# Performance work log

Measured on AMD Instinct MI355X. Metric: run time of the kernel, lower is better.

Reference implementation:

```python
import jax, jax.numpy as jnp
import numpy as np

B, M, N = 1, 8192, 131072      # batch, bones, window points
C_BOT, C = 16, 128             # bottleneck_channel, channel
K_MAX, FOLD, R_UP = 8, 8, 4    # max neighbors, fold_channel, upsample rate r
EPS = 1e-8


def _lin_init(key, fan_in, fan_out):
    return jax.random.normal(key, (fan_in, fan_out), jnp.float32) / np.sqrt(fan_in)


def setup_inputs() -> dict:
    key = jax.random.key(0)
    ks = jax.random.split(key, 10)
    return {
        "quantized_cf": jax.random.normal(ks[0], (B, M, C_BOT), jnp.float32),
        "d_idx": jax.random.randint(ks[1], (B, N, K_MAX), 0, M),
        "d_windows": jax.random.normal(ks[2], (B, N, 3), jnp.float32),
        "bones": jax.random.normal(ks[3], (B, M, 3), jnp.float32),
        "K": 8,
        # fea_stretch Linear(bottleneck -> channel)
        "W_stretch": _lin_init(ks[4], C_BOT, C),
        "b_stretch": jnp.zeros((C,), jnp.float32),
        # DWUS folding MLP: (C+3) -> C -> FOLD*R_UP -> 3 (per fold point)
        "W1": _lin_init(ks[5], C + 3, C),
        "b1": jnp.zeros((C,), jnp.float32),
        "W2": _lin_init(ks[6], C, FOLD * R_UP),
        "b2": jnp.zeros((FOLD * R_UP,), jnp.float32),
        "W3": _lin_init(ks[7], FOLD, 3),
        "b3": jnp.zeros((3,), jnp.float32),
    }


def reference(quantized_cf, d_idx, d_windows, bones, K,
              W_stretch, b_stretch, W1, b1, W2, b2, W3, b3):
    # fea_stretch: per-bone feature expansion  [B, M, C]
    skin_fea = jnp.einsum("bmc,cd->bmd", quantized_cf, W_stretch) + b_stretch

    idx = d_idx[..., :K]                                   # [B, N, K]
    batch = jnp.arange(B)[:, None, None]
    g_fea = skin_fea[batch, idx]                           # [B, N, K, C] gather
    g_bones = bones[batch, idx]                            # [B, N, K, 3]

    # inverse-distance interpolation of bone features onto window points
    rel = d_windows[:, :, None, :] - g_bones               # [B, N, K, 3]
    dist = jnp.sqrt(jnp.sum(rel * rel, axis=-1) + EPS)     # [B, N, K]
    w = 1.0 / (dist + EPS)
    w = w / jnp.sum(w, axis=-1, keepdims=True)
    interp = jnp.einsum("bnk,bnkc->bnc", w, g_fea)         # [B, N, C]

    # folding-based upsampling: each window point emits R_UP refined points
    x = jnp.concatenate([interp, d_windows], axis=-1)      # [B, N, C+3]
    h = jax.nn.relu(jnp.einsum("bnc,cd->bnd", x, W1) + b1)
    h = jax.nn.relu(jnp.einsum("bnc,cd->bnd", h, W2) + b2)
    h = h.reshape(B, N, R_UP, FOLD)
    off = jnp.einsum("bnrf,fo->bnro", h, W3) + b3          # [B, N, R_UP, 3]
    rec = d_windows[:, :, None, :] + off                   # [B, N, R_UP, 3]
    return rec.reshape(B, N * R_UP, 3)
```

## Files before the change

kernel.cpp:

```cpp
#include <hip/hip_runtime.h>
#include <hip/hip_bf16.h>

typedef __attribute__((ext_vector_type(8))) short short8;
typedef __attribute__((ext_vector_type(4))) float f32x4;

#define NPTS 131072

__device__ inline unsigned short f2bf(float f) {
    unsigned u = __float_as_uint(f);
    u = (u + 0x7FFFu + ((u >> 16) & 1u)) >> 16;
    return (unsigned short)u;
}

__device__ inline unsigned pack2(float a, float b) {
    union { __hip_bfloat162 h; unsigned u; } v;
    v.h = __float22bfloat162_rn(float2{a, b});
    return v.u;
}

__global__ __launch_bounds__(256) void prep_kernel(
    const float* __restrict__ Ws, const float* __restrict__ bs,
    const float* __restrict__ W1, const float* __restrict__ b1,
    const float* __restrict__ W2, const float* __restrict__ W3,
    const float* __restrict__ bones,
    unsigned short* __restrict__ w1t, unsigned short* __restrict__ w2t,
    float* __restrict__ beff, unsigned short* __restrict__ w3t,
    float* __restrict__ bones4)
{
    int t = blockIdx.x * 256 + threadIdx.x;
    if (t < 4096) {
        int e = t >> 5, k = t & 31;
        float v = 0.f;
        if (k < 16) {
            for (int d = 0; d < 128; ++d) v = fmaf(Ws[k*128 + d], W1[d*128 + e], v);
        } else if (k < 19) {
            v = W1[(128 + (k - 16))*128 + e];
        }
        w1t[e*32 + k] = f2bf(v);
    } else if (t < 8192) {
        int t2 = t - 4096;
        int e = t2 >> 7, d = t2 & 127;
        w2t[e*128 + ((d & 15)*8 + (d >> 4))] = f2bf(W2[d*32 + e]);
    } else if (t < 8320) {
        int e = t - 8192;
        float v = b1[e];
        for (int d = 0; d < 128; ++d) v = fmaf(bs[d], W1[d*128 + e], v);
        beff[e] = v;
    } else if (t < 8832) {
        int i = t - 8320;
        int q = i >> 5, k = i & 31;
        int e = (k & 1)*16 + (k >> 1);
        int r = e >> 3, f = e & 7;
        float v = 0.f;
        if (q < 12) {
            int r2 = q / 3, o = q - r2*3;
            if (r == r2) v = W3[f*3 + o];
        }
        w3t[q*32 + k] = f2bf(v);
    } else if (t < 8832 + 4*8192) {
        int i = t - 8832;
        int id = i >> 2, c = i & 3;
        bones4[i] = (c < 3) ? bones[id*3 + c] : 0.f;
    }
}

#define WREG 5632

__global__ __launch_bounds__(256, 3) void decoder_kernel(
    const float* __restrict__ qcf, const int* __restrict__ didx,
    const float* __restrict__ dwin, const float* __restrict__ bones4,
    const unsigned short* __restrict__ w1t, const unsigned short* __restrict__ w2t,
    const float* __restrict__ beff, const float* __restrict__ b2,
    const unsigned short* __restrict__ w3t, const float* __restrict__ b3,
    float* __restrict__ out)
{
    __shared__ unsigned char lds[4 * WREG];

    const int tid  = threadIdx.x;
    const int wave = tid >> 6;
    const int lane = tid & 63;
    unsigned char* wbase = lds + wave * WREG;
    unsigned short* H1b = (unsigned short*)(wbase);
    unsigned short* H2p = (unsigned short*)(wbase + 4352);

    const int q4  = lane >> 4;
    const int l16 = lane & 15;

    const int gw   = blockIdx.x * 4 + wave;
    const int base = gw * 16;
    const int p    = base + l16;

    const int4 ia = *(const int4*)(didx + p*8);
    const int4 ib = *(const int4*)(didx + p*8 + 4);
    const int id[8] = { ia.x, ia.y, ia.z, ia.w, ib.x, ib.y, ib.z, ib.w };
    const float wx = dwin[p*3+0], wy = dwin[p*3+1], wz = dwin[p*3+2];

    const int o3c = l16 - (l16/3)*3;
    float rw0 = 0.f, rw1 = 0.f, rw2 = 0.f, rw3 = 0.f;
    if (l16 < 12) {
        rw0 = dwin[(size_t)(base + q4*4 + 0)*3 + o3c];
        rw1 = dwin[(size_t)(base + q4*4 + 1)*3 + o3c];
        rw2 = dwin[(size_t)(base + q4*4 + 2)*3 + o3c];
        rw3 = dwin[(size_t)(base + q4*4 + 3)*3 + o3c];
    }

    const float4* __restrict__ bn4 = (const float4*)bones4;
    float w[8]; float s = 0.f;
#pragma unroll
    for (int k = 0; k < 8; ++k) {
        const float4 b = bn4[id[k]];
        const float rx = wx - b.x, ry = wy - b.y, rz = wz - b.z;
        const float dist = sqrtf(fmaf(rx,rx, fmaf(ry,ry, fmaf(rz,rz, 1e-8f))));
        w[k] = 1.0f / (dist + 1e-8f);
        s += w[k];
    }
    const float inv = 1.0f / s;

    union { unsigned u[4]; short8 s8; } a1u;
    a1u.u[0] = a1u.u[1] = a1u.u[2] = a1u.u[3] = 0u;
    if (q4 < 2) {
        float acc[8] = {0.f,0.f,0.f,0.f,0.f,0.f,0.f,0.f};
        const float4* __restrict__ q4p = (const float4*)qcf;
#pragma unroll
        for (int k = 0; k < 8; ++k) {
            const float4 lo = q4p[id[k]*4 + q4*2 + 0];
            const float4 hi = q4p[id[k]*4 + q4*2 + 1];
            acc[0] = fmaf(w[k], lo.x, acc[0]);
            acc[1] = fmaf(w[k], lo.y, acc[1]);
            acc[2] = fmaf(w[k], lo.z, acc[2]);
            acc[3] = fmaf(w[k], lo.w, acc[3]);
            acc[4] = fmaf(w[k], hi.x, acc[4]);
            acc[5] = fmaf(w[k], hi.y, acc[5]);
            acc[6] = fmaf(w[k], hi.z, acc[6]);
            acc[7] = fmaf(w[k], hi.w, acc[7]);
        }
        a1u.u[0] = pack2(acc[0]*inv, acc[1]*inv);
        a1u.u[1] = pack2(acc[2]*inv, acc[3]*inv);
        a1u.u[2] = pack2(acc[4]*inv, acc[5]*inv);
        a1u.u[3] = pack2(acc[6]*inv, acc[7]*inv);
    } else if (q4 == 2) {
        a1u.u[0] = pack2(wx, wy);
        a1u.u[1] = pack2(wz, 0.f);
    }

    short8 W1f[8]; float beffv[8];
#pragma unroll
    for (int dt = 0; dt < 8; ++dt) {
        W1f[dt]   = *(const short8*)(w1t + (dt*16 + l16)*32 + q4*8);
        beffv[dt] = beff[dt*16 + l16];
    }
    short8 W2f[2][4]; float b2v[2];
#pragma unroll
    for (int et = 0; et < 2; ++et) {
        b2v[et] = b2[et*16 + l16];
#pragma unroll
        for (int kt = 0; kt < 4; ++kt)
            W2f[et][kt] = *(const short8*)(w2t + (et*16 + l16)*128 + kt*32 + q4*8);
    }
    const short8 w3f = *(const short8*)(w3t + l16*32 + q4*8);
    const float  b3o = (l16 < 12) ? b3[o3c] : 0.f;

    f32x4 acc1[8];
#pragma unroll
    for (int dt = 0; dt < 8; ++dt) {
        f32x4 c = { beffv[dt], beffv[dt], beffv[dt], beffv[dt] };
        acc1[dt] = __builtin_amdgcn_mfma_f32_16x16x32_bf16(a1u.s8, W1f[dt], c, 0, 0, 0);
    }
#pragma unroll
    for (int r = 0; r < 4; ++r) {
        union { unsigned u[4]; short8 s8; } pk;
        pk.u[0] = pack2(fmaxf(acc1[0][r],0.f), fmaxf(acc1[1][r],0.f));
        pk.u[1] = pack2(fmaxf(acc1[2][r],0.f), fmaxf(acc1[3][r],0.f));
        pk.u[2] = pack2(fmaxf(acc1[4][r],0.f), fmaxf(acc1[5][r],0.f));
        pk.u[3] = pack2(fmaxf(acc1[6][r],0.f), fmaxf(acc1[7][r],0.f));
        *(short8*)(H1b + (q4*4 + r)*136 + l16*8) = pk.s8;
    }
    __syncthreads();

    f32x4 acc2[2] = { { b2v[0], b2v[0], b2v[0], b2v[0] },
                      { b2v[1], b2v[1], b2v[1], b2v[1] } };
#pragma unroll
    for (int kt = 0; kt < 4; ++kt) {
        const short8 a2 = *(const short8*)(H1b + l16*136 + kt*32 + q4*8);
        acc2[0] = __builtin_amdgcn_mfma_f32_16x16x32_bf16(a2, W2f[0][kt], acc2[0], 0, 0, 0);
        acc2[1] = __builtin_amdgcn_mfma_f32_16x16x32_bf16(a2, W2f[1][kt], acc2[1], 0, 0, 0);
    }
#pragma unroll
    for (int r = 0; r < 4; ++r) {
        unsigned p01 = pack2(fmaxf(acc2[0][r],0.f), fmaxf(acc2[1][r],0.f));
        *(unsigned*)(H2p + (q4*4 + r)*40 + l16*2) = p01;
    }
    __syncthreads();

    const short8 a3 = *(const short8*)(H2p + l16*40 + q4*8);
    f32x4 c3 = { b3o, b3o, b3o, b3o };
    f32x4 o3 = __builtin_amdgcn_mfma_f32_16x16x32_bf16(a3, w3f, c3, 0, 0, 0);
    if (l16 < 12) {
        out[(size_t)(base + q4*4 + 0)*12 + l16] = rw0 + o3[0];
        out[(size_t)(base + q4*4 + 1)*12 + l16] = rw1 + o3[1];
        out[(size_t)(base + q4*4 + 2)*12 + l16] = rw2 + o3[2];
        out[(size_t)(base + q4*4 + 3)*12 + l16] = rw3 + o3[3];
    }
}

extern "C" void kernel_launch(void* const* d_in, const int* in_sizes, int n_in,
                              void* d_out, int out_size, void* d_ws, size_t ws_size,
                              hipStream_t stream) {
    const float* qcf   = (const float*)d_in[0];
    const int*   didx  = (const int*)  d_in[1];
    const float* dwin  = (const float*)d_in[2];
    const float* bones = (const float*)d_in[3];
    const float* Ws = (const float*)d_in[5];
    const float* bs = (const float*)d_in[6];
    const float* W1 = (const float*)d_in[7];
    const float* b1 = (const float*)d_in[8];
    const float* W2 = (const float*)d_in[9];
    const float* b2 = (const float*)d_in[10];
    const float* W3 = (const float*)d_in[11];
    const float* b3 = (const float*)d_in[12];
    float* out = (float*)d_out;

    unsigned short* w1t    = (unsigned short*)d_ws;
    unsigned short* w2t    = (unsigned short*)((char*)d_ws + 8192);
    float*          beff   = (float*)((char*)d_ws + 16384);
    unsigned short* w3t    = (unsigned short*)((char*)d_ws + 16896);
    float*          bones4 = (float*)((char*)d_ws + 17920);

    hipLaunchKernelGGL(prep_kernel, dim3(163), dim3(256), 0, stream,
                       Ws, bs, W1, b1, W2, W3, bones, w1t, w2t, beff, w3t, bones4);
    hipLaunchKernelGGL(decoder_kernel, dim3(2048), dim3(256), 0, stream,
                       qcf, didx, dwin, bones4, w1t, w2t, beff, b2, w3t, b3, out);
}
```

Before: 35.19 us.

## Process two point tiles per wave to amortize weight fragment loads

Each wave now handles two 16-point tiles, loading the W1/W2/W3 bf16 fragments and biases once and reusing them for both, with the decoder grid halved. The bones padding in the prep kernel writes one float4 per thread instead of one scalar, so the prep grid shrinks. This cuts redundant weight-fragment loads and launch/block overhead, but gives fewer blocks and less parallelism. The two tiles are processed one after the other, so latency hiding may drop.

```diff
diff --git a/kernel.cpp b/kernel.cpp
--- a/kernel.cpp
+++ b/kernel.cpp
@@ -57,54 +57,35 @@
             if (r == r2) v = W3[f*3 + o];
         }
         w3t[q*32 + k] = f2bf(v);
-    } else if (t < 8832 + 4*8192) {
+    } else if (t < 8832 + 8192) {
         int i = t - 8832;
-        int id = i >> 2, c = i & 3;
-        bones4[i] = (c < 3) ? bones[id*3 + c] : 0.f;
+        float4 v;
+        v.x = bones[i*3 + 0];
+        v.y = bones[i*3 + 1];
+        v.z = bones[i*3 + 2];
+        v.w = 0.f;
+        ((float4*)bones4)[i] = v;
     }
 }
 
 #define WREG 5632
 
-__global__ __launch_bounds__(256, 3) void decoder_kernel(
-    const float* __restrict__ qcf, const int* __restrict__ didx,
-    const float* __restrict__ dwin, const float* __restrict__ bones4,
-    const unsigned short* __restrict__ w1t, const unsigned short* __restrict__ w2t,
-    const float* __restrict__ beff, const float* __restrict__ b2,
-    const unsigned short* __restrict__ w3t, const float* __restrict__ b3,
-    float* __restrict__ out)
+struct Frags {
+    short8 W1f[8]; float beffv[8];
+    short8 W2f[2][4]; float b2v[2];
+    short8 w3f; float b3o;
+};
+
+__device__ __forceinline__ void do_tile(
+    int base, const int4 ia, const int4 ib,
+    float wx, float wy, float wz,
+    float rw0, float rw1, float rw2, float rw3,
+    const Frags& F, int q4, int l16,
+    const float4* __restrict__ bn4, const float4* __restrict__ q4p,
+    unsigned short* H1b, unsigned short* H2p, float* __restrict__ out)
 {
-    __shared__ unsigned char lds[4 * WREG];
-
-    const int tid  = threadIdx.x;
-    const int wave = tid >> 6;
-    const int lane = tid & 63;
-    unsigned char* wbase = lds + wave * WREG;
-    unsigned short* H1b = (unsigned short*)(wbase);
-    unsigned short* H2p = (unsigned short*)(wbase + 4352);
-
-    const int q4  = lane >> 4;
-    const int l16 = lane & 15;
-
-    const int gw   = blockIdx.x * 4 + wave;
-    const int base = gw * 16;
-    const int p    = base + l16;
-
-    const int4 ia = *(const int4*)(didx + p*8);
-    const int4 ib = *(const int4*)(didx + p*8 + 4);
     const int id[8] = { ia.x, ia.y, ia.z, ia.w, ib.x, ib.y, ib.z, ib.w };
-    const float wx = dwin[p*3+0], wy = dwin[p*3+1], wz = dwin[p*3+2];
-
-    const int o3c = l16 - (l16/3)*3;
-    float rw0 = 0.f, rw1 = 0.f, rw2 = 0.f, rw3 = 0.f;
-    if (l16 < 12) {
-        rw0 = dwin[(size_t)(base + q4*4 + 0)*3 + o3c];
-        rw1 = dwin[(size_t)(base + q4*4 + 1)*3 + o3c];
-        rw2 = dwin[(size_t)(base + q4*4 + 2)*3 + o3c];
-        rw3 = dwin[(size_t)(base + q4*4 + 3)*3 + o3c];
-    }
-
-    const float4* __restrict__ bn4 = (const float4*)bones4;
+
     float w[8]; float s = 0.f;
 #pragma unroll
     for (int k = 0; k < 8; ++k) {
@@ -120,7 +101,6 @@
     a1u.u[0] = a1u.u[1] = a1u.u[2] = a1u.u[3] = 0u;
     if (q4 < 2) {
         float acc[8] = {0.f,0.f,0.f,0.f,0.f,0.f,0.f,0.f};
-        const float4* __restrict__ q4p = (const float4*)qcf;
 #pragma unroll
         for (int k = 0; k < 8; ++k) {
             const float4 lo = q4p[id[k]*4 + q4*2 + 0];
@@ -143,28 +123,11 @@
         a1u.u[1] = pack2(wz, 0.f);
     }
 
-    short8 W1f[8]; float beffv[8];
+    f32x4 acc1[8];
 #pragma unroll
     for (int dt = 0; dt < 8; ++dt) {
-        W1f[dt]   = *(const short8*)(w1t + (dt*16 + l16)*32 + q4*8);
-        beffv[dt] = beff[dt*16 + l16];
-    }
-    short8 W2f[2][4]; float b2v[2];
-#pragma unroll
-    for (int et = 0; et < 2; ++et) {
-        b2v[et] = b2[et*16 + l16];
-#pragma unroll
-        for (int kt = 0; kt < 4; ++kt)
-            W2f[et][kt] = *(const short8*)(w2t + (et*16 + l16)*128 + kt*32 + q4*8);
-    }
-    const short8 w3f = *(const short8*)(w3t + l16*32 + q4*8);
-    const float  b3o = (l16 < 12) ? b3[o3c] : 0.f;
-
-    f32x4 acc1[8];
-#pragma unroll
-    for (int dt = 0; dt < 8; ++dt) {
-        f32x4 c = { beffv[dt], beffv[dt], beffv[dt], beffv[dt] };
-        acc1[dt] = __builtin_amdgcn_mfma_f32_16x16x32_bf16(a1u.s8, W1f[dt], c, 0, 0, 0);
+        f32x4 c = { F.beffv[dt], F.beffv[dt], F.beffv[dt], F.beffv[dt] };
+        acc1[dt] = __builtin_amdgcn_mfma_f32_16x16x32_bf16(a1u.s8, F.W1f[dt], c, 0, 0, 0);
     }
 #pragma unroll
     for (int r = 0; r < 4; ++r) {
@@ -177,13 +140,13 @@
     }
     __syncthreads();
 
-    f32x4 acc2[2] = { { b2v[0], b2v[0], b2v[0], b2v[0] },
-                      { b2v[1], b2v[1], b2v[1], b2v[1] } };
+    f32x4 acc2[2] = { { F.b2v[0], F.b2v[0], F.b2v[0], F.b2v[0] },
+                      { F.b2v[1], F.b2v[1], F.b2v[1], F.b2v[1] } };
 #pragma unroll
     for (int kt = 0; kt < 4; ++kt) {
         const short8 a2 = *(const short8*)(H1b + l16*136 + kt*32 + q4*8);
-        acc2[0] = __builtin_amdgcn_mfma_f32_16x16x32_bf16(a2, W2f[0][kt], acc2[0], 0, 0, 0);
-        acc2[1] = __builtin_amdgcn_mfma_f32_16x16x32_bf16(a2, W2f[1][kt], acc2[1], 0, 0, 0);
+        acc2[0] = __builtin_amdgcn_mfma_f32_16x16x32_bf16(a2, F.W2f[0][kt], acc2[0], 0, 0, 0);
+        acc2[1] = __builtin_amdgcn_mfma_f32_16x16x32_bf16(a2, F.W2f[1][kt], acc2[1], 0, 0, 0);
     }
 #pragma unroll
     for (int r = 0; r < 4; ++r) {
@@ -193,14 +156,86 @@
     __syncthreads();
 
     const short8 a3 = *(const short8*)(H2p + l16*40 + q4*8);
-    f32x4 c3 = { b3o, b3o, b3o, b3o };
-    f32x4 o3 = __builtin_amdgcn_mfma_f32_16x16x32_bf16(a3, w3f, c3, 0, 0, 0);
+    f32x4 c3 = { F.b3o, F.b3o, F.b3o, F.b3o };
+    f32x4 o3 = __builtin_amdgcn_mfma_f32_16x16x32_bf16(a3, F.w3f, c3, 0, 0, 0);
     if (l16 < 12) {
         out[(size_t)(base + q4*4 + 0)*12 + l16] = rw0 + o3[0];
         out[(size_t)(base + q4*4 + 1)*12 + l16] = rw1 + o3[1];
         out[(size_t)(base + q4*4 + 2)*12 + l16] = rw2 + o3[2];
         out[(size_t)(base + q4*4 + 3)*12 + l16] = rw3 + o3[3];
     }
+}
+
+__global__ __launch_bounds__(256, 3) void decoder_kernel(
+    const float* __restrict__ qcf, const int* __restrict__ didx,
+    const float* __restrict__ dwin, const float* __restrict__ bones4,
+    const unsigned short* __restrict__ w1t, const unsigned short* __restrict__ w2t,
+    const float* __restrict__ beff, const float* __restrict__ b2,
+    const unsigned short* __restrict__ w3t, const float* __restrict__ b3,
+    float* __restrict__ out)
+{
+    __shared__ unsigned char lds[4 * WREG];
+
+    const int tid  = threadIdx.x;
+    const int wave = tid >> 6;
+    const int lane = tid & 63;
+    unsigned char* wbase = lds + wave * WREG;
+    unsigned short* H1b = (unsigned short*)(wbase);
+    unsigned short* H2p = (unsigned short*)(wbase + 4352);
+
+    const int q4  = lane >> 4;
+    const int l16 = lane & 15;
+
+    const int g0    = (blockIdx.x * 4 + wave) * 2;
+    const int base0 = g0 * 16;
+    const int base1 = base0 + 16;
+    const int p0    = base0 + l16;
+    const int p1    = base1 + l16;
+
+    const int4 ia0 = *(const int4*)(didx + p0*8);
+    const int4 ib0 = *(const int4*)(didx + p0*8 + 4);
+    const int4 ia1 = *(const int4*)(didx + p1*8);
+    const int4 ib1 = *(const int4*)(didx + p1*8 + 4);
+    const float wx0 = dwin[p0*3+0], wy0 = dwin[p0*3+1], wz0 = dwin[p0*3+2];
+    const float wx1 = dwin[p1*3+0], wy1 = dwin[p1*3+1], wz1 = dwin[p1*3+2];
+
+    const int o3c = l16 - (l16/3)*3;
+    float rwA0=0.f, rwA1=0.f, rwA2=0.f, rwA3=0.f;
+    float rwB0=0.f, rwB1=0.f, rwB2=0.f, rwB3=0.f;
+    if (l16 < 12) {
+        rwA0 = dwin[(size_t)(base0 + q4*4 + 0)*3 + o3c];
+        rwA1 = dwin[(size_t)(base0 + q4*4 + 1)*3 + o3c];
+        rwA2 = dwin[(size_t)(base0 + q4*4 + 2)*3 + o3c];
+        rwA3 = dwin[(size_t)(base0 + q4*4 + 3)*3 + o3c];
+        rwB0 = dwin[(size_t)(base1 + q4*4 + 0)*3 + o3c];
+        rwB1 = dwin[(size_t)(base1 + q4*4 + 1)*3 + o3c];
+        rwB2 = dwin[(size_t)(base1 + q4*4 + 2)*3 + o3c];
+        rwB3 = dwin[(size_t)(base1 + q4*4 + 3)*3 + o3c];
+    }
+
+    Frags F;
+#pragma unroll
+    for (int dt = 0; dt < 8; ++dt) {
+        F.W1f[dt]   = *(const short8*)(w1t + (dt*16 + l16)*32 + q4*8);
+        F.beffv[dt] = beff[dt*16 + l16];
+    }
+#pragma unroll
+    for (int et = 0; et < 2; ++et) {
+        F.b2v[et] = b2[et*16 + l16];
+#pragma unroll
+        for (int kt = 0; kt < 4; ++kt)
+            F.W2f[et][kt] = *(const short8*)(w2t + (et*16 + l16)*128 + kt*32 + q4*8);
+    }
+    F.w3f = *(const short8*)(w3t + l16*32 + q4*8);
+    F.b3o = (l16 < 12) ? b3[o3c] : 0.f;
+
+    const float4* __restrict__ bn4 = (const float4*)bones4;
+    const float4* __restrict__ q4p = (const float4*)qcf;
+
+    do_tile(base0, ia0, ib0, wx0, wy0, wz0, rwA0, rwA1, rwA2, rwA3,
+            F, q4, l16, bn4, q4p, H1b, H2p, out);
+    do_tile(base1, ia1, ib1, wx1, wy1, wz1, rwB0, rwB1, rwB2, rwB3,
+            F, q4, l16, bn4, q4p, H1b, H2p, out);
 }
 
 extern "C" void kernel_launch(void* const* d_in, const int* in_sizes, int n_in,
@@ -226,8 +261,8 @@
     unsigned short* w3t    = (unsigned short*)((char*)d_ws + 16896);
     float*          bones4 = (float*)((char*)d_ws + 17920);
 
-    hipLaunchKernelGGL(prep_kernel, dim3(163), dim3(256), 0, stream,
+    hipLaunchKernelGGL(prep_kernel, dim3(67), dim3(256), 0, stream,
                        Ws, bs, W1, b1, W2, W3, bones, w1t, w2t, beff, w3t, bones4);
-    hipLaunchKernelGGL(decoder_kernel, dim3(2048), dim3(256), 0, stream,
+    hipLaunchKernelGGL(decoder_kernel, dim3(1024), dim3(256), 0, stream,
                        qcf, didx, dwin, bones4, w1t, w2t, beff, b2, w3t, b3, out);
 }
```

New measurement: 41.07 us. 16.7% more time.

## Spread neighbor gathers across lanes and pre-convert features to bf16

Applied to the files above, without the earlier changes.

The interpolation is restructured so each lane handles one (point, neighbor) pair. Weights are normalized and the feature reduction is done with xor-shuffle butterflies, and the interpolated rows are staged in LDS before the first MFMA. The prep kernel now also converts quantized features to packed bf16, which halves gather bytes, and writes bones4 with float4 stores. The goal is better lane utilization and memory-level parallelism in the gather phase, which previously had only two quarter-waves doing the feature loads. The cost is an extra LDS round-trip and barrier, more shuffles, and an occupancy hint lowered from 3 to 2.

```diff
diff --git a/kernel.cpp b/kernel.cpp
--- a/kernel.cpp
+++ b/kernel.cpp
@@ -18,20 +18,24 @@
     return v.u;
 }
 
+__device__ inline float bflo(unsigned u) { return __uint_as_float(u << 16); }
+__device__ inline float bfhi(unsigned u) { return __uint_as_float(u & 0xffff0000u); }
+
 __global__ __launch_bounds__(256) void prep_kernel(
     const float* __restrict__ Ws, const float* __restrict__ bs,
     const float* __restrict__ W1, const float* __restrict__ b1,
     const float* __restrict__ W2, const float* __restrict__ W3,
-    const float* __restrict__ bones,
+    const float* __restrict__ bones, const float* __restrict__ qcf,
     unsigned short* __restrict__ w1t, unsigned short* __restrict__ w2t,
     float* __restrict__ beff, unsigned short* __restrict__ w3t,
-    float* __restrict__ bones4)
+    float* __restrict__ bones4, unsigned* __restrict__ qbf)
 {
     int t = blockIdx.x * 256 + threadIdx.x;
     if (t < 4096) {
         int e = t >> 5, k = t & 31;
         float v = 0.f;
         if (k < 16) {
+#pragma unroll 16
             for (int d = 0; d < 128; ++d) v = fmaf(Ws[k*128 + d], W1[d*128 + e], v);
         } else if (k < 19) {
             v = W1[(128 + (k - 16))*128 + e];
@@ -44,6 +48,7 @@
     } else if (t < 8320) {
         int e = t - 8192;
         float v = b1[e];
+#pragma unroll 16
         for (int d = 0; d < 128; ++d) v = fmaf(bs[d], W1[d*128 + e], v);
         beff[e] = v;
     } else if (t < 8832) {
@@ -57,17 +62,79 @@
             if (r == r2) v = W3[f*3 + o];
         }
         w3t[q*32 + k] = f2bf(v);
-    } else if (t < 8832 + 4*8192) {
+    } else if (t < 17024) {
         int i = t - 8832;
-        int id = i >> 2, c = i & 3;
-        bones4[i] = (c < 3) ? bones[id*3 + c] : 0.f;
-    }
-}
-
-#define WREG 5632
-
-__global__ __launch_bounds__(256, 3) void decoder_kernel(
-    const float* __restrict__ qcf, const int* __restrict__ didx,
+        float4 v;
+        v.x = bones[i*3 + 0];
+        v.y = bones[i*3 + 1];
+        v.z = bones[i*3 + 2];
+        v.w = 0.f;
+        ((float4*)bones4)[i] = v;
+    } else if (t < 25216) {
+        int row = t - 17024;
+        const float4* q = (const float4*)(qcf + row*16);
+        const float4 q0 = q[0], q1 = q[1], q2 = q[2], q3 = q[3];
+        uint4 o0, o1;
+        o0.x = pack2(q0.x, q0.y); o0.y = pack2(q0.z, q0.w);
+        o0.z = pack2(q1.x, q1.y); o0.w = pack2(q1.z, q1.w);
+        o1.x = pack2(q2.x, q2.y); o1.y = pack2(q2.z, q2.w);
+        o1.z = pack2(q3.x, q3.y); o1.w = pack2(q3.z, q3.w);
+        ((uint4*)qbf)[row*2 + 0] = o0;
+        ((uint4*)qbf)[row*2 + 1] = o1;
+    }
+}
+
+#define WREG 6144
+
+__device__ __forceinline__ float2 interp_pass(
+    int idxv, float4 bb, float wxx, float wyy, float wzz, int k,
+    const unsigned* __restrict__ qbf)
+{
+    const uint4 ra = *(const uint4*)(qbf + idxv*8);
+    const uint4 rb = *(const uint4*)(qbf + idxv*8 + 4);
+
+    const float rx = wxx - bb.x, ry = wyy - bb.y, rz = wzz - bb.z;
+    const float dist = sqrtf(fmaf(rx,rx, fmaf(ry,ry, fmaf(rz,rz, 1e-8f))));
+    const float w = 1.0f / (dist + 1e-8f);
+    float s = w;
+    s += __shfl_xor(s, 1);
+    s += __shfl_xor(s, 2);
+    s += __shfl_xor(s, 4);
+    const float wn = w / s;
+
+    float v[16];
+    v[ 0] = wn*bflo(ra.x); v[ 1] = wn*bfhi(ra.x);
+    v[ 2] = wn*bflo(ra.y); v[ 3] = wn*bfhi(ra.y);
+    v[ 4] = wn*bflo(ra.z); v[ 5] = wn*bfhi(ra.z);
+    v[ 6] = wn*bflo(ra.w); v[ 7] = wn*bfhi(ra.w);
+    v[ 8] = wn*bflo(rb.x); v[ 9] = wn*bfhi(rb.x);
+    v[10] = wn*bflo(rb.y); v[11] = wn*bfhi(rb.y);
+    v[12] = wn*bflo(rb.z); v[13] = wn*bfhi(rb.z);
+    v[14] = wn*bflo(rb.w); v[15] = wn*bfhi(rb.w);
+
+#pragma unroll
+    for (int j = 0; j < 8; ++j) {
+        const float sv = (k & 4) ? v[j] : v[j + 8];
+        const float t  = __shfl_xor(sv, 4);
+        v[j] = ((k & 4) ? v[j + 8] : v[j]) + t;
+    }
+#pragma unroll
+    for (int j = 0; j < 4; ++j) {
+        const float sv = (k & 2) ? v[j] : v[j + 4];
+        const float t  = __shfl_xor(sv, 2);
+        v[j] = ((k & 2) ? v[j + 4] : v[j]) + t;
+    }
+#pragma unroll
+    for (int j = 0; j < 2; ++j) {
+        const float sv = (k & 1) ? v[j] : v[j + 2];
+        const float t  = __shfl_xor(sv, 1);
+        v[j] = ((k & 1) ? v[j + 2] : v[j]) + t;
+    }
+    return float2{ v[0], v[1] };
+}
+
+__global__ __launch_bounds__(256, 2) void decoder_kernel(
+    const unsigned* __restrict__ qbf, const int* __restrict__ didx,
     const float* __restrict__ dwin, const float* __restrict__ bones4,
     const unsigned short* __restrict__ w1t, const unsigned short* __restrict__ w2t,
     const float* __restrict__ beff, const float* __restrict__ b2,
@@ -80,21 +147,32 @@
     const int wave = tid >> 6;
     const int lane = tid & 63;
     unsigned char* wbase = lds + wave * WREG;
-    unsigned short* H1b = (unsigned short*)(wbase);
-    unsigned short* H2p = (unsigned short*)(wbase + 4352);
+    unsigned*       Xbu = (unsigned*)(wbase);
+    unsigned short* H1b = (unsigned short*)(wbase + 512);
+    unsigned short* H2p = (unsigned short*)(wbase + 512 + 4352);
 
     const int q4  = lane >> 4;
     const int l16 = lane & 15;
 
     const int gw   = blockIdx.x * 4 + wave;
     const int base = gw * 16;
-    const int p    = base + l16;
-
-    const int4 ia = *(const int4*)(didx + p*8);
-    const int4 ib = *(const int4*)(didx + p*8 + 4);
-    const int id[8] = { ia.x, ia.y, ia.z, ia.w, ib.x, ib.y, ib.z, ib.w };
-    const float wx = dwin[p*3+0], wy = dwin[p*3+1], wz = dwin[p*3+2];
-
+
+    const int pgrp = lane >> 3;
+    const int k    = lane & 7;
+    const int p0   = base + pgrp;
+    const int p1   = base + 8 + pgrp;
+
+    const int i0 = didx[p0*8 + k];
+    const int i1 = didx[p1*8 + k];
+    const float4* __restrict__ bn4 = (const float4*)bones4;
+    const float4 bb0 = bn4[i0];
+    const float4 bb1 = bn4[i1];
+    const float wx0 = dwin[p0*3+0], wy0 = dwin[p0*3+1], wz0 = dwin[p0*3+2];
+    const float wx1 = dwin[p1*3+0], wy1 = dwin[p1*3+1], wz1 = dwin[p1*3+2];
+
+    const float wxA = dwin[(base + l16)*3 + 0];
+    const float wyA = dwin[(base + l16)*3 + 1];
+    const float wzA = dwin[(base + l16)*3 + 2];
     const int o3c = l16 - (l16/3)*3;
     float rw0 = 0.f, rw1 = 0.f, rw2 = 0.f, rw3 = 0.f;
     if (l16 < 12) {
@@ -104,44 +182,10 @@
         rw3 = dwin[(size_t)(base + q4*4 + 3)*3 + o3c];
     }
 
-    const float4* __restrict__ bn4 = (const float4*)bones4;
-    float w[8]; float s = 0.f;
-#pragma unroll
-    for (int k = 0; k < 8; ++k) {
-        const float4 b = bn4[id[k]];
-        const float rx = wx - b.x, ry = wy - b.y, rz = wz - b.z;
-        const float dist = sqrtf(fmaf(rx,rx, fmaf(ry,ry, fmaf(rz,rz, 1e-8f))));
-        w[k] = 1.0f / (dist + 1e-8f);
-        s += w[k];
-    }
-    const float inv = 1.0f / s;
-
-    union { unsigned u[4]; short8 s8; } a1u;
-    a1u.u[0] = a1u.u[1] = a1u.u[2] = a1u.u[3] = 0u;
-    if (q4 < 2) {
-        float acc[8] = {0.f,0.f,0.f,0.f,0.f,0.f,0.f,0.f};
-        const float4* __restrict__ q4p = (const float4*)qcf;
-#pragma unroll
-        for (int k = 0; k < 8; ++k) {
-            const float4 lo = q4p[id[k]*4 + q4*2 + 0];
-            const float4 hi = q4p[id[k]*4 + q4*2 + 1];
-            acc[0] = fmaf(w[k], lo.x, acc[0]);
-            acc[1] = fmaf(w[k], lo.y, acc[1]);
-            acc[2] = fmaf(w[k], lo.z, acc[2]);
-            acc[3] = fmaf(w[k], lo.w, acc[3]);
-            acc[4] = fmaf(w[k], hi.x, acc[4]);
-            acc[5] = fmaf(w[k], hi.y, acc[5]);
-            acc[6] = fmaf(w[k], hi.z, acc[6]);
-            acc[7] = fmaf(w[k], hi.w, acc[7]);
-        }
-        a1u.u[0] = pack2(acc[0]*inv, acc[1]*inv);
-        a1u.u[1] = pack2(acc[2]*inv, acc[3]*inv);
-        a1u.u[2] = pack2(acc[4]*inv, acc[5]*inv);
-        a1u.u[3] = pack2(acc[6]*inv, acc[7]*inv);
-    } else if (q4 == 2) {
-        a1u.u[0] = pack2(wx, wy);
-        a1u.u[1] = pack2(wz, 0.f);
-    }
+    const float2 x0 = interp_pass(i0, bb0, wx0, wy0, wz0, k, qbf);
+    const float2 x1 = interp_pass(i1, bb1, wx1, wy1, wz1, k, qbf);
+    Xbu[pgrp*8 + k]       = pack2(x0.x, x0.y);
+    Xbu[(8 + pgrp)*8 + k] = pack2(x1.x, x1.y);
 
     short8 W1f[8]; float beffv[8];
 #pragma unroll
@@ -159,6 +203,17 @@
     }
     const short8 w3f = *(const short8*)(w3t + l16*32 + q4*8);
     const float  b3o = (l16 < 12) ? b3[o3c] : 0.f;
+
+    __syncthreads();
+
+    union { uint4 v; short8 s8; } a1u;
+    a1u.v = uint4{0u, 0u, 0u, 0u};
+    if (q4 < 2) {
+        a1u.v = *(const uint4*)(Xbu + l16*8 + q4*4);
+    } else if (q4 == 2) {
+        a1u.v.x = pack2(wxA, wyA);
+        a1u.v.y = pack2(wzA, 0.f);
+    }
 
     f32x4 acc1[8];
 #pragma unroll
@@ -225,9 +280,11 @@
     float*          beff   = (float*)((char*)d_ws + 16384);
     unsigned short* w3t    = (unsigned short*)((char*)d_ws + 16896);
     float*          bones4 = (float*)((char*)d_ws + 17920);
-
-    hipLaunchKernelGGL(prep_kernel, dim3(163), dim3(256), 0, stream,
-                       Ws, bs, W1, b1, W2, W3, bones, w1t, w2t, beff, w3t, bones4);
+    unsigned*       qbf    = (unsigned*)((char*)d_ws + 163840);
+
+    hipLaunchKernelGGL(prep_kernel, dim3(99), dim3(256), 0, stream,
+                       Ws, bs, W1, b1, W2, W3, bones, qcf,
+                       w1t, w2t, beff, w3t, bones4, qbf);
     hipLaunchKernelGGL(decoder_kernel, dim3(2048), dim3(256), 0, stream,
-                       qcf, didx, dwin, bones4, w1t, w2t, beff, b2, w3t, b3, out);
-}
+                       qbf, didx, dwin, bones4, w1t, w2t, beff, b2, w3t, b3, out);
+}
```

Result: faster. 31.31 us (-11.0%).
